# Optimization experiments

Measured on AMD Instinct MI355X. Metric: run time of the kernel, lower is better.

Reference implementation:

```python
import jax, jax.numpy as jnp
import numpy as np

E, D, H = 1024, 64, 16   # embed_dim, head_dim, num_heads
B, L = 8, 4096


def _ln(x, g, b, eps=1e-5):
    m = jnp.mean(x, axis=-1, keepdims=True)
    v = jnp.var(x, axis=-1, keepdims=True)
    return (x - m) / jnp.sqrt(v + eps) * g + b


def setup_inputs() -> dict:
    key = jax.random.key(0)
    ks = jax.random.split(key, 10)
    s_e = 1.0 / np.sqrt(E)
    s_d = 1.0 / np.sqrt(D)
    f32 = jnp.float32
    return {
        "emb": jax.random.normal(ks[0], (B, L, E), f32),
        # per-head linears stacked on a leading head axis
        "Wa": jax.random.normal(ks[1], (H, E, D), f32) * s_e,
        "ba": jnp.zeros((H, D), f32),
        "Wb": jax.random.normal(ks[2], (H, E, D), f32) * s_e,
        "bb": jnp.zeros((H, D), f32),
        "Wc": jax.random.normal(ks[3], (H, D, D), f32) * s_d,
        "bc": jnp.zeros((H, D), f32),
        "head_w": jnp.ones((H,), f32),
        "hn_g": jnp.ones((H, D), f32),
        "hn_b": jnp.zeros((H, D), f32),
        "Wd": jax.random.normal(ks[4], (E, D), f32) * s_e,
        "bd": jnp.zeros((D,), f32),
        "W1": jax.random.normal(ks[5], (D, 4 * D), f32) * s_d,
        "b1": jnp.zeros((4 * D,), f32),
        "W2": jax.random.normal(ks[6], (4 * D, D), f32) * (1.0 / np.sqrt(4 * D)),
        "b2": jnp.zeros((D,), f32),
        "Wp": jax.random.normal(ks[7], (D, D), f32) * s_d,
        "bp": jnp.zeros((D,), f32),
        "ng": jnp.ones((D,), f32),
        "nb": jnp.zeros((D,), f32),
    }


def reference(emb, Wa, ba, Wb, bb, Wc, bc, head_w, hn_g, hn_b,
              Wd, bd, W1, b1, W2, b2, Wp, bp, ng, nb):
    b_sz, seq_len, _ = emb.shape
    n_heads, d_head = ba.shape

    # gates depend only on x_t -> precompute for all t, all heads  [B,L,H,D]
    a = jnp.tanh(jnp.einsum('ble,hed->blhd', emb, Wa) + ba)
    bt = jnp.einsum('ble,hed->blhd', emb, Wb) + bb

    # linear recurrence h_t = a_t * h_{t-1} + b_t over time
    a_t = jnp.moveaxis(a, 1, 0)    # [L,B,H,D]
    b_t = jnp.moveaxis(bt, 1, 0)

    def step(h, ab):
        at, btt = ab
        h = at * h + btt
        return h, h

    h0 = jnp.zeros((b_sz, n_heads, d_head), emb.dtype)
    _, hs = jax.lax.scan(step, h0, (a_t, b_t))
    hs = jnp.moveaxis(hs, 0, 1)    # [B,L,H,D]

    dx = emb @ Wd + bd             # [B,L,D] shared D(x_t)

    out = jnp.einsum('blhd,hde->blhe', hs, Wc) + bc + dx[:, :, None, :]
    out = _ln(out, hn_g, hn_b)     # per-head LayerNorm, gamma/beta [H,D]

    sum_heads = dx + jnp.einsum('h,blhd->bld', head_w, out)
    z = sum_heads / n_heads

    u = z + _ln(z, ng, nb)
    ffn = jax.nn.gelu(u @ W1 + b1, approximate=False) @ W2 + b2
    h_out = u + ffn
    return h_out @ Wp + bp
```

## Files before the change

kernel.cpp:

```cpp
#include <hip/hip_runtime.h>
#include <hip/hip_bf16.h>
#include <math.h>
#include <stdint.h>

#define E_DIM 1024
#define D_DIM 64
#define H_DIM 16
#define B_SZ  8
#define L_SEQ 4096
#define M_TOK (B_SZ * L_SEQ)
#define NCAT  2112
#define NPAD  2304
#define CHUNK 64
#define NCHUNK (L_SEQ / CHUNK)

typedef float  f32x4  __attribute__((ext_vector_type(4)));
typedef __bf16 bf16x8 __attribute__((ext_vector_type(8)));
typedef __bf16 bf16x4 __attribute__((ext_vector_type(4)));

__device__ __forceinline__ float tanh_fast(float v) {
  float vc = fminf(fmaxf(v, -12.f), 12.f);
  float ex = __expf(vc + vc);
  return (ex - 1.f) / (ex + 1.f);
}
__device__ __forceinline__ void load_lds16(const void* g, void* l) {
  __builtin_amdgcn_global_load_lds(
      (const __attribute__((address_space(1))) void*)g,
      (__attribute__((address_space(3))) void*)l, 16, 0, 0);
}

__global__ __launch_bounds__(256) void cast_emb(const float* __restrict__ in,
                                                bf16x4* __restrict__ out) {
  int i = blockIdx.x * 256 + threadIdx.x;
  float4 v = ((const float4*)in)[i];
  bf16x4 o;
  o[0] = (__bf16)v.x; o[1] = (__bf16)v.y; o[2] = (__bf16)v.z; o[3] = (__bf16)v.w;
  out[i] = o;
}

__global__ __launch_bounds__(256) void pack_w(
    const float* __restrict__ Wa, const float* __restrict__ ba,
    const float* __restrict__ Wb, const float* __restrict__ bb,
    const float* __restrict__ Wd, const float* __restrict__ bd,
    __bf16* __restrict__ wcat, float* __restrict__ bias) {
  int gid = blockIdx.x * 256 + threadIdx.x;
  int n = gid >> 10, e = gid & 1023;
  int nt = n >> 8, c = n & 255;
  float w, bv;
  if (nt < 8) {
    int k = nt * 128 + (c >> 1);
    int h = k >> 6, d = k & 63;
    if ((c & 1) == 0) { w = Wa[((h << 10) | e) * 64 + d]; bv = ba[k]; }
    else              { w = Wb[((h << 10) | e) * 64 + d]; bv = bb[k]; }
  } else {
    if (c < 64) { w = Wd[e * 64 + c]; bv = bd[c]; }
    else        { w = 0.f; bv = 0.f; }
  }
  wcat[n * 1024 + e] = (__bf16)w;
  if (e == 0) bias[n] = bv;
}

__global__ __launch_bounds__(256) void pack_ffnw(
    const float* __restrict__ W1, const float* __restrict__ W2,
    const float* __restrict__ Wp,
    __bf16* __restrict__ g_w1t, __bf16* __restrict__ g_w2t,
    __bf16* __restrict__ g_wpt) {
  int idx = blockIdx.x * 256 + threadIdx.x;
  if (idx < 16384) {
    int k = idx >> 8, n = idx & 255;
    g_w1t[n * 72 + k] = (__bf16)W1[idx];
  } else if (idx < 32768) {
    int j = idx - 16384; int k = j >> 6, n = j & 63;
    g_w2t[n * 256 + (((k >> 3) ^ (n & 7)) << 3) + (k & 7)] = (__bf16)W2[j];
  } else {
    int j = idx - 32768; int k = j >> 6, n = j & 63;
    g_wpt[n * 72 + k] = (__bf16)Wp[j];
  }
}

__global__ __launch_bounds__(256) void pack_wct(const float* __restrict__ Wc,
                                                __bf16* __restrict__ wct) {
  int idx = blockIdx.x * 256 + threadIdx.x;
  int h = idx >> 12, e = (idx >> 6) & 63, d = idx & 63;
  wct[idx] = (__bf16)Wc[h * 4096 + d * 64 + e];
}

__global__ __launch_bounds__(512) void gemm_scan_fused(
    const __bf16* __restrict__ A, const __bf16* __restrict__ Wt,
    const float* __restrict__ bias,
    __bf16* __restrict__ abuf, __bf16* __restrict__ bbuf, float* __restrict__ dxbuf,
    float* __restrict__ cA, float* __restrict__ cH) {
  __shared__ __bf16 lds[34816];
  const int id = blockIdx.x;
  const int wg = (id & 7) * 144 + (id >> 3);
  const int mt = wg / 9, nt = wg % 9;
  const int m0 = mt * 256, n0 = nt * 256;
  const int t = threadIdx.x;
  const int w = t >> 6, l = t & 63;
  const int wr = w >> 2, wc = w & 3;
  const int q = l >> 4, c16 = l & 15;
  const int cp = q ^ ((c16 >> 1) & 3);

  f32x4 acc[8][4];
#pragma unroll
  for (int i = 0; i < 8; ++i)
#pragma unroll
    for (int j = 0; j < 4; ++j) acc[i][j] = (f32x4)(0.f);

  auto stage = [&](int kt) {
    const int s = kt & 1;
#pragma unroll
    for (int i = 0; i < 2; ++i) {
      int li = i * 512 + t;
      int rr = li >> 2;
      int lc = (li & 3) ^ ((rr >> 1) & 3);
      load_lds16(A + (size_t)(m0 + rr) * 1024 + kt * 32 + lc * 8,
                 (char*)lds + s * 32768 + li * 16);
      load_lds16(Wt + (size_t)(n0 + rr) * 1024 + kt * 32 + lc * 8,
                 (char*)lds + s * 32768 + 16384 + li * 16);
    }
  };

  stage(0); stage(1);
#pragma unroll 2
  for (int tt = 0; tt < 32; ++tt) {
    if (tt < 31) { asm volatile("s_waitcnt vmcnt(4)" ::: "memory"); }
    else         { asm volatile("s_waitcnt vmcnt(0)" ::: "memory"); }
    __builtin_amdgcn_s_barrier();
    __builtin_amdgcn_sched_barrier(0);
    const __bf16* Abase = lds + (tt & 1) * 16384;
    const __bf16* Bbase = Abase + 8192;
    bf16x8 bfr[4];
#pragma unroll
    for (int j = 0; j < 4; ++j)
      bfr[j] = *(const bf16x8*)(Bbase + (wc * 64 + j * 16 + c16) * 32 + cp * 8);
#pragma unroll
    for (int i = 0; i < 8; ++i) {
      bf16x8 af = *(const bf16x8*)(Abase + (wr * 128 + i * 16 + c16) * 32 + cp * 8);
#pragma unroll
      for (int j = 0; j < 4; ++j)
        acc[i][j] = __builtin_amdgcn_mfma_f32_16x16x32_bf16(af, bfr[j], acc[i][j], 0, 0, 0);
    }
    __builtin_amdgcn_sched_barrier(0);
    __builtin_amdgcn_s_barrier();
    __builtin_amdgcn_sched_barrier(0);
    if (tt < 30) stage(tt + 2);
  }

  const int cbase = m0 >> 6;
  if (nt < 8) {
    float bv4[4];
#pragma unroll
    for (int j = 0; j < 4; ++j) bv4[j] = bias[n0 + wc * 64 + j * 16 + c16];
#pragma unroll 1
    for (int ph = 0; ph < 2; ++ph) {
      __syncthreads();
      if ((wc >> 1) == ph) {
#pragma unroll
        for (int j = 0; j < 4; ++j) {
          int cl = (wc & 1) * 64 + j * 16 + c16;
#pragma unroll
          for (int i = 0; i < 8; ++i) {
            int rowb = wr * 128 + i * 16 + q * 4;
#pragma unroll
            for (int r = 0; r < 4; ++r) {
              float v = acc[i][j][r] + bv4[j];
              float val = (c16 & 1) ? v : tanh_fast(v);
              *(__bf16*)((char*)lds + (rowb + r) * 272 + cl * 2) = (__bf16)val;
            }
          }
        }
      }
      __syncthreads();
      if (t < 256) {
        const int c4 = t >> 6, pp = t & 63;
        const int gk = nt * 128 + ph * 64 + pp;
        const int rb = c4 * 64;
        float p = 1.f, h = 0.f;
        size_t g = (size_t)(m0 + rb) * 1024 + gk;
        const char* lrow = (const char*)lds + rb * 272 + pp * 4;
#pragma unroll 4
        for (int st = 0; st < 64; ++st) {
          float a = (float)*(const __bf16*)(lrow);
          float b = (float)*(const __bf16*)(lrow + 2);
          lrow += 272;
          p *= a;
          h = fmaf(a, h, b);
          abuf[g] = (__bf16)p;
          bbuf[g] = (__bf16)h;
          g += 1024;
        }
        int ci = (cbase + c4) * 1024 + gk;
        cA[ci] = p; cH[ci] = h;
      }
    }
  } else {
    if (wc == 0) {
      float bv4[4];
#pragma unroll
      for (int j = 0; j < 4; ++j) bv4[j] = bias[n0 + j * 16 + c16];
#pragma unroll
      for (int j = 0; j < 4; ++j) {
        int e = j * 16 + c16;
#pragma unroll
        for (int i = 0; i < 8; ++i) {
          int rowb = m0 + wr * 128 + i * 16 + q * 4;
#pragma unroll
          for (int r = 0; r < 4; ++r)
            dxbuf[(size_t)(rowb + r) * 64 + e] = acc[i][j][r] + bv4[j];
        }
      }
    }
  }
}

__global__ __launch_bounds__(256) void scan_carry(
    const float* __restrict__ cA, const float* __restrict__ cH, float* __restrict__ cIn) {
  int gid = blockIdx.x * 256 + threadIdx.x;
  int n = gid & 1023, b = gid >> 10;
  float carry = 0.f;
  for (int c = 0; c < NCHUNK; ++c) {
    int idx = (b * NCHUNK + c) * 1024 + n;
    cIn[idx] = carry;
    carry = fmaf(cA[idx], carry, cH[idx]);
  }
}

__global__ __launch_bounds__(256) void heads_mfma(
    const __bf16* __restrict__ ahat, const __bf16* __restrict__ hloc,
    const float* __restrict__ dxbuf, const float* __restrict__ cIn,
    const __bf16* __restrict__ wct, const float* __restrict__ bch,
    const float* __restrict__ head_w, const float* __restrict__ hng,
    const float* __restrict__ hnb, const float* __restrict__ ng,
    const float* __restrict__ nbv, float* __restrict__ ubuf) {
  __shared__ float carryS[1024];
  const int tid = threadIdx.x, w = tid >> 6, l = tid & 63;
  const int q = l >> 4, c16 = l & 15;
  const int m0 = blockIdx.x * 64;
  const int b = m0 >> 12, c = (m0 & 4095) >> 6;
  const int cb = (b * NCHUNK + c) * 1024;
  ((float4*)carryS)[tid] = ((const float4*)(cIn + cb))[tid];
  __syncthreads();

  const size_t arow = (size_t)(m0 + w * 16 + c16) * 1024;

  float dxr[4][4];
#pragma unroll
  for (int j = 0; j < 4; ++j)
#pragma unroll
    for (int r = 0; r < 4; ++r)
      dxr[j][r] = dxbuf[(m0 + w * 16 + q * 4 + r) * 64 + j * 16 + c16];

  f32x4 accum[4];
#pragma unroll
  for (int j = 0; j < 4; ++j) accum[j] = (f32x4)(0.f);

  for (int h = 0; h < H_DIM; ++h) {
    bf16x8 af[2];
#pragma unroll
    for (int ks = 0; ks < 2; ++ks) {
      int dbase = h * 64 + ks * 32 + q * 8;
      bf16x8 av = *(const bf16x8*)(ahat + arow + dbase);
      bf16x8 hv = *(const bf16x8*)(hloc + arow + dbase);
      float4 cv0 = *(const float4*)(carryS + dbase);
      float4 cv1 = *(const float4*)(carryS + dbase + 4);
      bf16x8 hf;
      hf[0] = (__bf16)fmaf((float)av[0], cv0.x, (float)hv[0]);
      hf[1] = (__bf16)fmaf((float)av[1], cv0.y, (float)hv[1]);
      hf[2] = (__bf16)fmaf((float)av[2], cv0.z, (float)hv[2]);
      hf[3] = (__bf16)fmaf((float)av[3], cv0.w, (float)hv[3]);
      hf[4] = (__bf16)fmaf((float)av[4], cv1.x, (float)hv[4]);
      hf[5] = (__bf16)fmaf((float)av[5], cv1.y, (float)hv[5]);
      hf[6] = (__bf16)fmaf((float)av[6], cv1.z, (float)hv[6]);
      hf[7] = (__bf16)fmaf((float)av[7], cv1.w, (float)hv[7]);
      af[ks] = hf;
    }
    f32x4 acc[4];
#pragma unroll
    for (int j = 0; j < 4; ++j) acc[j] = (f32x4)(0.f);
#pragma unroll
    for (int ks = 0; ks < 2; ++ks)
#pragma unroll
      for (int j = 0; j < 4; ++j) {
        bf16x8 bf = *(const bf16x8*)(wct + h * 4096 + (j * 16 + c16) * 64 + ks * 32 + q * 8);
        acc[j] = __builtin_amdgcn_mfma_f32_16x16x32_bf16(af[ks], bf, acc[j], 0, 0, 0);
      }
    float hw = head_w[h];
    float g4[4], be4[4], bb4[4];
#pragma unroll
    for (int j = 0; j < 4; ++j) {
      int nh = h * 64 + j * 16 + c16;
      g4[j] = hng[nh]; bb4[j] = hnb[nh]; be4[j] = bch[nh];
    }
#pragma unroll
    for (int r = 0; r < 4; ++r) {
      float v0 = acc[0][r] + be4[0] + dxr[0][r];
      float v1 = acc[1][r] + be4[1] + dxr[1][r];
      float v2 = acc[2][r] + be4[2] + dxr[2][r];
      float v3 = acc[3][r] + be4[3] + dxr[3][r];
      float s  = (v0 + v1) + (v2 + v3);
      float s2 = fmaf(v0, v0, fmaf(v1, v1, fmaf(v2, v2, v3 * v3)));
#pragma unroll
      for (int off = 1; off < 16; off <<= 1) {
        s  += __shfl_xor(s, off, 64);
        s2 += __shfl_xor(s2, off, 64);
      }
      float mean = s * (1.f / 64.f);
      float var  = fmaf(s2, 1.f / 64.f, -mean * mean);
      float inv  = rsqrtf(fmaxf(var, 0.f) + 1e-5f);
      accum[0][r] = fmaf(hw, fmaf((v0 - mean) * inv, g4[0], bb4[0]), accum[0][r]);
      accum[1][r] = fmaf(hw, fmaf((v1 - mean) * inv, g4[1], bb4[1]), accum[1][r]);
      accum[2][r] = fmaf(hw, fmaf((v2 - mean) * inv, g4[2], bb4[2]), accum[2][r]);
      accum[3][r] = fmaf(hw, fmaf((v3 - mean) * inv, g4[3], bb4[3]), accum[3][r]);
    }
  }
  float ng4[4], nb4[4];
#pragma unroll
  for (int j = 0; j < 4; ++j) { ng4[j] = ng[j * 16 + c16]; nb4[j] = nbv[j * 16 + c16]; }
#pragma unroll
  for (int r = 0; r < 4; ++r) {
    float z0 = (dxr[0][r] + accum[0][r]) * (1.f / 16.f);
    float z1 = (dxr[1][r] + accum[1][r]) * (1.f / 16.f);
    float z2 = (dxr[2][r] + accum[2][r]) * (1.f / 16.f);
    float z3 = (dxr[3][r] + accum[3][r]) * (1.f / 16.f);
    float s  = (z0 + z1) + (z2 + z3);
    float s2 = fmaf(z0, z0, fmaf(z1, z1, fmaf(z2, z2, z3 * z3)));
#pragma unroll
    for (int off = 1; off < 16; off <<= 1) {
      s  += __shfl_xor(s, off, 64);
      s2 += __shfl_xor(s2, off, 64);
    }
    float mean = s * (1.f / 64.f);
    float var  = fmaf(s2, 1.f / 64.f, -mean * mean);
    float inv  = rsqrtf(fmaxf(var, 0.f) + 1e-5f);
    int mrow = (m0 + w * 16 + q * 4 + r) * 64;
    ubuf[mrow + 0 * 16 + c16] = z0 + fmaf((z0 - mean) * inv, ng4[0], nb4[0]);
    ubuf[mrow + 1 * 16 + c16] = z1 + fmaf((z1 - mean) * inv, ng4[1], nb4[1]);
    ubuf[mrow + 2 * 16 + c16] = z2 + fmaf((z2 - mean) * inv, ng4[2], nb4[2]);
    ubuf[mrow + 3 * 16 + c16] = z3 + fmaf((z3 - mean) * inv, ng4[3], nb4[3]);
  }
}

__global__ __launch_bounds__(256) void ffn_mfma(
    const float* __restrict__ ubuf,
    const __bf16* __restrict__ g_w1t, const __bf16* __restrict__ g_w2t,
    const __bf16* __restrict__ g_wpt,
    const float* __restrict__ b1, const float* __restrict__ b2,
    const float* __restrict__ bp, float* __restrict__ out) {
  __shared__ __bf16 pool[32768];
  const int tid = threadIdx.x, w = tid >> 6, l = tid & 63;
  const int q = l >> 4, c16 = l & 15;
  const int m0 = blockIdx.x * 64;
  __bf16* Us  = pool;
  __bf16* W1T = pool + 4608;
  __bf16* T1S = pool;
  __bf16* W2T = pool + 16384;
  __bf16* HoS = pool;
  __bf16* WpT = pool + 4608;

#pragma unroll
  for (int r = 0; r < 16; ++r) {
    int idx = r * 256 + tid, m = idx >> 6, e = idx & 63;
    Us[m * 72 + e] = (__bf16)ubuf[(size_t)(m0 + m) * 64 + e];
  }
#pragma unroll
  for (int r = 0; r < 9; ++r)
    load_lds16(g_w1t + (size_t)(r * 256 + tid) * 8,
               (char*)pool + 9216 + (r * 256 + w * 64) * 16);
  __syncthreads();

  f32x4 acc1[16];
#pragma unroll
  for (int j = 0; j < 16; ++j) acc1[j] = (f32x4)(0.f);
#pragma unroll
  for (int ks = 0; ks < 2; ++ks) {
    bf16x8 a = *(const bf16x8*)(Us + (w * 16 + c16) * 72 + ks * 32 + q * 8);
#pragma unroll
    for (int j = 0; j < 16; ++j) {
      bf16x8 b = *(const bf16x8*)(W1T + (j * 16 + c16) * 72 + ks * 32 + q * 8);
      acc1[j] = __builtin_amdgcn_mfma_f32_16x16x32_bf16(a, b, acc1[j], 0, 0, 0);
    }
  }
  __syncthreads();

#pragma unroll
  for (int r = 0; r < 8; ++r)
    load_lds16(g_w2t + (size_t)(r * 256 + tid) * 8,
               (char*)pool + 32768 + (r * 256 + w * 64) * 16);
#pragma unroll
  for (int j = 0; j < 16; ++j) {
    int n = j * 16 + c16;
    float bv = b1[n];
#pragma unroll
    for (int rr = 0; rr < 4; ++rr) {
      int m = w * 16 + q * 4 + rr;
      float x = acc1[j][rr] + bv;
      float g = 0.5f * x * (1.f + erff(x * 0.70710678118654752f));
      T1S[m * 256 + (((n >> 3) ^ (m & 7)) << 3) + (n & 7)] = (__bf16)g;
    }
  }
  __syncthreads();

  f32x4 acc2[4];
#pragma unroll
  for (int j = 0; j < 4; ++j) acc2[j] = (f32x4)(0.f);
  const int arow2 = w * 16 + c16;
#pragma unroll
  for (int ks = 0; ks < 8; ++ks) {
    bf16x8 a = *(const bf16x8*)(T1S + arow2 * 256 + (((ks * 4 + q) ^ (arow2 & 7)) << 3));
#pragma unroll
    for (int j = 0; j < 4; ++j) {
      int brow = j * 16 + c16;
      bf16x8 b = *(const bf16x8*)(W2T + brow * 256 + (((ks * 4 + q) ^ (brow & 7)) << 3));
      acc2[j] = __builtin_amdgcn_mfma_f32_16x16x32_bf16(a, b, acc2[j], 0, 0, 0);
    }
  }
  __syncthreads();

#pragma unroll
  for (int r = 0; r < 2; ++r)
    load_lds16(g_wpt + (size_t)(r * 256 + tid) * 8,
               (char*)pool + 9216 + (r * 256 + w * 64) * 16);
  if (tid < 64)
    load_lds16(g_wpt + (size_t)(512 + tid) * 8, (char*)pool + 9216 + 512 * 16);
#pragma unroll
  for (int j = 0; j < 4; ++j) {
    int e = j * 16 + c16;
    float bv = b2[e];
#pragma unroll
    for (int rr = 0; rr < 4; ++rr) {
      int m = w * 16 + q * 4 + rr;
      float hres = acc2[j][rr] + bv + ubuf[(size_t)(m0 + m) * 64 + e];
      HoS[m * 72 + e] = (__bf16)hres;
    }
  }
  __syncthreads();

  f32x4 acc3[4];
#pragma unroll
  for (int j = 0; j < 4; ++j) acc3[j] = (f32x4)(0.f);
#pragma unroll
  for (int ks = 0; ks < 2; ++ks) {
    bf16x8 a = *(const bf16x8*)(HoS + (w * 16 + c16) * 72 + ks * 32 + q * 8);
#pragma unroll
    for (int j = 0; j < 4; ++j) {
      bf16x8 b = *(const bf16x8*)(WpT + (j * 16 + c16) * 72 + ks * 32 + q * 8);
      acc3[j] = __builtin_amdgcn_mfma_f32_16x16x32_bf16(a, b, acc3[j], 0, 0, 0);
    }
  }
#pragma unroll
  for (int j = 0; j < 4; ++j) {
    int e = j * 16 + c16;
    float bv = bp[e];
#pragma unroll
    for (int rr = 0; rr < 4; ++rr) {
      int m = w * 16 + q * 4 + rr;
      out[(size_t)(m0 + m) * 64 + e] = acc3[j][rr] + bv;
    }
  }
}

extern "C" void kernel_launch(void* const* d_in, const int* in_sizes, int n_in,
                              void* d_out, int out_size, void* d_ws, size_t ws_size,
                              hipStream_t stream) {
  const float* emb    = (const float*)d_in[0];
  const float* Wa     = (const float*)d_in[1];
  const float* ba     = (const float*)d_in[2];
  const float* Wb     = (const float*)d_in[3];
  const float* bb     = (const float*)d_in[4];
  const float* Wc     = (const float*)d_in[5];
  const float* bc     = (const float*)d_in[6];
  const float* head_w = (const float*)d_in[7];
  const float* hn_g   = (const float*)d_in[8];
  const float* hn_b   = (const float*)d_in[9];
  const float* Wd     = (const float*)d_in[10];
  const float* bd     = (const float*)d_in[11];
  const float* W1     = (const float*)d_in[12];
  const float* b1     = (const float*)d_in[13];
  const float* W2     = (const float*)d_in[14];
  const float* b2     = (const float*)d_in[15];
  const float* Wp     = (const float*)d_in[16];
  const float* bp     = (const float*)d_in[17];
  const float* ng     = (const float*)d_in[18];
  const float* nb     = (const float*)d_in[19];
  float* out = (float*)d_out;

  char* wsp = (char*)d_ws;
  size_t off = 0;
  auto alloc = [&](size_t bytes) -> char* {
    char* p = wsp + off;
    off += (bytes + 255) & ~(size_t)255;
    return p;
  };
  __bf16* embh  = (__bf16*)alloc((size_t)M_TOK * E_DIM * 2);
  __bf16* wcat  = (__bf16*)alloc((size_t)NPAD * E_DIM * 2);
  float*  bias  = (float*)alloc((size_t)NPAD * 4);
  __bf16* abuf  = (__bf16*)alloc((size_t)M_TOK * 1024 * 2);
  __bf16* bbuf  = (__bf16*)alloc((size_t)M_TOK * 1024 * 2);
  float*  dxbuf = (float*)alloc((size_t)M_TOK * 64 * 4);
  float*  cA    = (float*)alloc((size_t)512 * 1024 * 4);
  float*  cH    = (float*)alloc((size_t)512 * 1024 * 4);
  float*  cIn   = (float*)alloc((size_t)512 * 1024 * 4);
  float*  ubuf  = (float*)alloc((size_t)M_TOK * 64 * 4);
  __bf16* g_w1t = (__bf16*)alloc((size_t)256 * 72 * 2);
  __bf16* g_w2t = (__bf16*)alloc((size_t)64 * 256 * 2);
  __bf16* g_wpt = (__bf16*)alloc((size_t)64 * 72 * 2);
  __bf16* wct   = (__bf16*)alloc((size_t)H_DIM * 64 * 64 * 2);

  cast_emb<<<dim3(32768), dim3(256), 0, stream>>>(emb, (bf16x4*)embh);
  pack_w<<<dim3(9216), dim3(256), 0, stream>>>(Wa, ba, Wb, bb, Wd, bd, wcat, bias);
  pack_ffnw<<<dim3(144), dim3(256), 0, stream>>>(W1, W2, Wp, g_w1t, g_w2t, g_wpt);
  pack_wct<<<dim3(256), dim3(256), 0, stream>>>(Wc, wct);
  gemm_scan_fused<<<dim3(1152), dim3(512), 0, stream>>>(embh, wcat, bias, abuf, bbuf,
                                                        dxbuf, cA, cH);
  scan_carry<<<dim3(32), dim3(256), 0, stream>>>(cA, cH, cIn);
  heads_mfma<<<dim3(512), dim3(256), 0, stream>>>(abuf, bbuf, dxbuf, cIn, wct, bc,
                                                  head_w, hn_g, hn_b, ng, nb, ubuf);
  ffn_mfma<<<dim3(512), dim3(256), 0, stream>>>(ubuf, g_w1t, g_w2t, g_wpt,
                                                b1, b2, bp, out);
}
```

Baseline: 562.5 us.

## Fuse heads and FFN kernels, merge weight packing, batch carry-scan loads

```diff
diff --git a/kernel.cpp b/kernel.cpp
--- a/kernel.cpp
+++ b/kernel.cpp
@@ -38,51 +38,51 @@
   out[i] = o;
 }
 
-__global__ __launch_bounds__(256) void pack_w(
+#define PK0 (NPAD * 1024)
+#define PK1 36864
+#define PK2 65536
+__global__ __launch_bounds__(256) void pack_all(
     const float* __restrict__ Wa, const float* __restrict__ ba,
     const float* __restrict__ Wb, const float* __restrict__ bb,
     const float* __restrict__ Wd, const float* __restrict__ bd,
-    __bf16* __restrict__ wcat, float* __restrict__ bias) {
+    const float* __restrict__ W1, const float* __restrict__ W2,
+    const float* __restrict__ Wp, const float* __restrict__ Wc,
+    __bf16* __restrict__ wcat, float* __restrict__ bias,
+    __bf16* __restrict__ g_w1t, __bf16* __restrict__ g_w2t,
+    __bf16* __restrict__ g_wpt, __bf16* __restrict__ wct) {
   int gid = blockIdx.x * 256 + threadIdx.x;
-  int n = gid >> 10, e = gid & 1023;
-  int nt = n >> 8, c = n & 255;
-  float w, bv;
-  if (nt < 8) {
-    int k = nt * 128 + (c >> 1);
-    int h = k >> 6, d = k & 63;
-    if ((c & 1) == 0) { w = Wa[((h << 10) | e) * 64 + d]; bv = ba[k]; }
-    else              { w = Wb[((h << 10) | e) * 64 + d]; bv = bb[k]; }
+  if (gid < PK0) {
+    int n = gid >> 10, e = gid & 1023;
+    int nt = n >> 8, c = n & 255;
+    float w, bv;
+    if (nt < 8) {
+      int k = nt * 128 + (c >> 1);
+      int h = k >> 6, d = k & 63;
+      if ((c & 1) == 0) { w = Wa[((h << 10) | e) * 64 + d]; bv = ba[k]; }
+      else              { w = Wb[((h << 10) | e) * 64 + d]; bv = bb[k]; }
+    } else {
+      if (c < 64) { w = Wd[e * 64 + c]; bv = bd[c]; }
+      else        { w = 0.f; bv = 0.f; }
+    }
+    wcat[n * 1024 + e] = (__bf16)w;
+    if (e == 0) bias[n] = bv;
+  } else if (gid < PK0 + PK1) {
+    int idx = gid - PK0;
+    if (idx < 16384) {
+      int k = idx >> 8, n = idx & 255;
+      g_w1t[n * 72 + k] = (__bf16)W1[idx];
+    } else if (idx < 32768) {
+      int j = idx - 16384; int k = j >> 6, n = j & 63;
+      g_w2t[n * 256 + (((k >> 3) ^ (n & 7)) << 3) + (k & 7)] = (__bf16)W2[j];
+    } else {
+      int j = idx - 32768; int k = j >> 6, n = j & 63;
+      g_wpt[n * 72 + k] = (__bf16)Wp[j];
+    }
   } else {
-    if (c < 64) { w = Wd[e * 64 + c]; bv = bd[c]; }
-    else        { w = 0.f; bv = 0.f; }
-  }
-  wcat[n * 1024 + e] = (__bf16)w;
-  if (e == 0) bias[n] = bv;
-}
-
-__global__ __launch_bounds__(256) void pack_ffnw(
-    const float* __restrict__ W1, const float* __restrict__ W2,
-    const float* __restrict__ Wp,
-    __bf16* __restrict__ g_w1t, __bf16* __restrict__ g_w2t,
-    __bf16* __restrict__ g_wpt) {
-  int idx = blockIdx.x * 256 + threadIdx.x;
-  if (idx < 16384) {
-    int k = idx >> 8, n = idx & 255;
-    g_w1t[n * 72 + k] = (__bf16)W1[idx];
-  } else if (idx < 32768) {
-    int j = idx - 16384; int k = j >> 6, n = j & 63;
-    g_w2t[n * 256 + (((k >> 3) ^ (n & 7)) << 3) + (k & 7)] = (__bf16)W2[j];
-  } else {
-    int j = idx - 32768; int k = j >> 6, n = j & 63;
-    g_wpt[n * 72 + k] = (__bf16)Wp[j];
-  }
-}
-
-__global__ __launch_bounds__(256) void pack_wct(const float* __restrict__ Wc,
-                                                __bf16* __restrict__ wct) {
-  int idx = blockIdx.x * 256 + threadIdx.x;
-  int h = idx >> 12, e = (idx >> 6) & 63, d = idx & 63;
-  wct[idx] = (__bf16)Wc[h * 4096 + d * 64 + e];
+    int idx = gid - PK0 - PK1;
+    int h = idx >> 12, e = (idx >> 6) & 63, d = idx & 63;
+    wct[idx] = (__bf16)Wc[h * 4096 + d * 64 + e];
+  }
 }
 
 __global__ __launch_bounds__(512) void gemm_scan_fused(
@@ -218,25 +218,52 @@
     const float* __restrict__ cA, const float* __restrict__ cH, float* __restrict__ cIn) {
   int gid = blockIdx.x * 256 + threadIdx.x;
   int n = gid & 1023, b = gid >> 10;
+  const int base = b * NCHUNK * 1024 + n;
   float carry = 0.f;
-  for (int c = 0; c < NCHUNK; ++c) {
-    int idx = (b * NCHUNK + c) * 1024 + n;
-    cIn[idx] = carry;
-    carry = fmaf(cA[idx], carry, cH[idx]);
-  }
-}
-
-__global__ __launch_bounds__(256) void heads_mfma(
+#pragma unroll 1
+  for (int c0 = 0; c0 < NCHUNK; c0 += 8) {
+    float a8[8], h8[8];
+#pragma unroll
+    for (int i = 0; i < 8; ++i) {
+      int idx = base + (c0 + i) * 1024;
+      a8[i] = cA[idx]; h8[i] = cH[idx];
+    }
+#pragma unroll
+    for (int i = 0; i < 8; ++i) {
+      cIn[base + (c0 + i) * 1024] = carry;
+      carry = fmaf(a8[i], carry, h8[i]);
+    }
+  }
+}
+
+__global__ __launch_bounds__(256) void heads_ffn(
     const __bf16* __restrict__ ahat, const __bf16* __restrict__ hloc,
     const float* __restrict__ dxbuf, const float* __restrict__ cIn,
     const __bf16* __restrict__ wct, const float* __restrict__ bch,
     const float* __restrict__ head_w, const float* __restrict__ hng,
     const float* __restrict__ hnb, const float* __restrict__ ng,
-    const float* __restrict__ nbv, float* __restrict__ ubuf) {
-  __shared__ float carryS[1024];
+    const float* __restrict__ nbv,
+    const __bf16* __restrict__ g_w1t, const __bf16* __restrict__ g_w2t,
+    const __bf16* __restrict__ g_wpt,
+    const float* __restrict__ b1, const float* __restrict__ b2,
+    const float* __restrict__ bp, float* __restrict__ out) {
+  __shared__ __bf16 pool[32768];
+  float* carryS = (float*)pool;
   const int tid = threadIdx.x, w = tid >> 6, l = tid & 63;
   const int q = l >> 4, c16 = l & 15;
   const int m0 = blockIdx.x * 64;
+  __bf16* Us  = pool;
+  __bf16* W1T = pool + 4608;
+  __bf16* T1S = pool;
+  __bf16* W2T = pool + 16384;
+  __bf16* HoS = pool;
+  __bf16* WpT = pool + 4608;
+
+#pragma unroll
+  for (int r = 0; r < 9; ++r)
+    load_lds16(g_w1t + (size_t)(r * 256 + tid) * 8,
+               (char*)pool + 9216 + (r * 256 + w * 64) * 16);
+
   const int b = m0 >> 12, c = (m0 & 4095) >> 6;
   const int cb = (b * NCHUNK + c) * 1024;
   ((float4*)carryS)[tid] = ((const float4*)(cIn + cb))[tid];
@@ -314,6 +341,7 @@
       accum[3][r] = fmaf(hw, fmaf((v3 - mean) * inv, g4[3], bb4[3]), accum[3][r]);
     }
   }
+  float u4[4][4];
   float ng4[4], nb4[4];
 #pragma unroll
   for (int j = 0; j < 4; ++j) { ng4[j] = ng[j * 16 + c16]; nb4[j] = nbv[j * 16 + c16]; }
@@ -333,40 +361,17 @@
     float mean = s * (1.f / 64.f);
     float var  = fmaf(s2, 1.f / 64.f, -mean * mean);
     float inv  = rsqrtf(fmaxf(var, 0.f) + 1e-5f);
-    int mrow = (m0 + w * 16 + q * 4 + r) * 64;
-    ubuf[mrow + 0 * 16 + c16] = z0 + fmaf((z0 - mean) * inv, ng4[0], nb4[0]);
-    ubuf[mrow + 1 * 16 + c16] = z1 + fmaf((z1 - mean) * inv, ng4[1], nb4[1]);
-    ubuf[mrow + 2 * 16 + c16] = z2 + fmaf((z2 - mean) * inv, ng4[2], nb4[2]);
-    ubuf[mrow + 3 * 16 + c16] = z3 + fmaf((z3 - mean) * inv, ng4[3], nb4[3]);
-  }
-}
-
-__global__ __launch_bounds__(256) void ffn_mfma(
-    const float* __restrict__ ubuf,
-    const __bf16* __restrict__ g_w1t, const __bf16* __restrict__ g_w2t,
-    const __bf16* __restrict__ g_wpt,
-    const float* __restrict__ b1, const float* __restrict__ b2,
-    const float* __restrict__ bp, float* __restrict__ out) {
-  __shared__ __bf16 pool[32768];
-  const int tid = threadIdx.x, w = tid >> 6, l = tid & 63;
-  const int q = l >> 4, c16 = l & 15;
-  const int m0 = blockIdx.x * 64;
-  __bf16* Us  = pool;
-  __bf16* W1T = pool + 4608;
-  __bf16* T1S = pool;
-  __bf16* W2T = pool + 16384;
-  __bf16* HoS = pool;
-  __bf16* WpT = pool + 4608;
-
-#pragma unroll
-  for (int r = 0; r < 16; ++r) {
-    int idx = r * 256 + tid, m = idx >> 6, e = idx & 63;
-    Us[m * 72 + e] = (__bf16)ubuf[(size_t)(m0 + m) * 64 + e];
-  }
-#pragma unroll
-  for (int r = 0; r < 9; ++r)
-    load_lds16(g_w1t + (size_t)(r * 256 + tid) * 8,
-               (char*)pool + 9216 + (r * 256 + w * 64) * 16);
+    u4[0][r] = z0 + fmaf((z0 - mean) * inv, ng4[0], nb4[0]);
+    u4[1][r] = z1 + fmaf((z1 - mean) * inv, ng4[1], nb4[1]);
+    u4[2][r] = z2 + fmaf((z2 - mean) * inv, ng4[2], nb4[2]);
+    u4[3][r] = z3 + fmaf((z3 - mean) * inv, ng4[3], nb4[3]);
+  }
+  __syncthreads();
+#pragma unroll
+  for (int j = 0; j < 4; ++j)
+#pragma unroll
+    for (int r = 0; r < 4; ++r)
+      Us[(w * 16 + q * 4 + r) * 72 + j * 16 + c16] = (__bf16)u4[j][r];
   __syncthreads();
 
   f32x4 acc1[16];
@@ -377,8 +382,8 @@
     bf16x8 a = *(const bf16x8*)(Us + (w * 16 + c16) * 72 + ks * 32 + q * 8);
 #pragma unroll
     for (int j = 0; j < 16; ++j) {
-      bf16x8 b = *(const bf16x8*)(W1T + (j * 16 + c16) * 72 + ks * 32 + q * 8);
-      acc1[j] = __builtin_amdgcn_mfma_f32_16x16x32_bf16(a, b, acc1[j], 0, 0, 0);
+      bf16x8 bfr = *(const bf16x8*)(W1T + (j * 16 + c16) * 72 + ks * 32 + q * 8);
+      acc1[j] = __builtin_amdgcn_mfma_f32_16x16x32_bf16(a, bfr, acc1[j], 0, 0, 0);
     }
   }
   __syncthreads();
@@ -411,8 +416,8 @@
 #pragma unroll
     for (int j = 0; j < 4; ++j) {
       int brow = j * 16 + c16;
-      bf16x8 b = *(const bf16x8*)(W2T + brow * 256 + (((ks * 4 + q) ^ (brow & 7)) << 3));
-      acc2[j] = __builtin_amdgcn_mfma_f32_16x16x32_bf16(a, b, acc2[j], 0, 0, 0);
+      bf16x8 bfr = *(const bf16x8*)(W2T + brow * 256 + (((ks * 4 + q) ^ (brow & 7)) << 3));
+      acc2[j] = __builtin_amdgcn_mfma_f32_16x16x32_bf16(a, bfr, acc2[j], 0, 0, 0);
     }
   }
   __syncthreads();
@@ -430,7 +435,7 @@
 #pragma unroll
     for (int rr = 0; rr < 4; ++rr) {
       int m = w * 16 + q * 4 + rr;
-      float hres = acc2[j][rr] + bv + ubuf[(size_t)(m0 + m) * 64 + e];
+      float hres = acc2[j][rr] + bv + u4[j][rr];
       HoS[m * 72 + e] = (__bf16)hres;
     }
   }
@@ -444,8 +449,8 @@
     bf16x8 a = *(const bf16x8*)(HoS + (w * 16 + c16) * 72 + ks * 32 + q * 8);
 #pragma unroll
     for (int j = 0; j < 4; ++j) {
-      bf16x8 b = *(const bf16x8*)(WpT + (j * 16 + c16) * 72 + ks * 32 + q * 8);
-      acc3[j] = __builtin_amdgcn_mfma_f32_16x16x32_bf16(a, b, acc3[j], 0, 0, 0);
+      bf16x8 bfr = *(const bf16x8*)(WpT + (j * 16 + c16) * 72 + ks * 32 + q * 8);
+      acc3[j] = __builtin_amdgcn_mfma_f32_16x16x32_bf16(a, bfr, acc3[j], 0, 0, 0);
     }
   }
 #pragma unroll
@@ -501,21 +506,20 @@
   float*  cA    = (float*)alloc((size_t)512 * 1024 * 4);
   float*  cH    = (float*)alloc((size_t)512 * 1024 * 4);
   float*  cIn   = (float*)alloc((size_t)512 * 1024 * 4);
-  float*  ubuf  = (float*)alloc((size_t)M_TOK * 64 * 4);
   __bf16* g_w1t = (__bf16*)alloc((size_t)256 * 72 * 2);
   __bf16* g_w2t = (__bf16*)alloc((size_t)64 * 256 * 2);
   __bf16* g_wpt = (__bf16*)alloc((size_t)64 * 72 * 2);
   __bf16* wct   = (__bf16*)alloc((size_t)H_DIM * 64 * 64 * 2);
 
   cast_emb<<<dim3(32768), dim3(256), 0, stream>>>(emb, (bf16x4*)embh);
-  pack_w<<<dim3(9216), dim3(256), 0, stream>>>(Wa, ba, Wb, bb, Wd, bd, wcat, bias);
-  pack_ffnw<<<dim3(144), dim3(256), 0, stream>>>(W1, W2, Wp, g_w1t, g_w2t, g_wpt);
-  pack_wct<<<dim3(256), dim3(256), 0, stream>>>(Wc, wct);
+  pack_all<<<dim3(9616), dim3(256), 0, stream>>>(Wa, ba, Wb, bb, Wd, bd,
+                                                 W1, W2, Wp, Wc,
+                                                 wcat, bias, g_w1t, g_w2t, g_wpt, wct);
   gemm_scan_fused<<<dim3(1152), dim3(512), 0, stream>>>(embh, wcat, bias, abuf, bbuf,
                                                         dxbuf, cA, cH);
   scan_carry<<<dim3(32), dim3(256), 0, stream>>>(cA, cH, cIn);
-  heads_mfma<<<dim3(512), dim3(256), 0, stream>>>(abuf, bbuf, dxbuf, cIn, wct, bc,
-                                                  head_w, hn_g, hn_b, ng, nb, ubuf);
-  ffn_mfma<<<dim3(512), dim3(256), 0, stream>>>(ubuf, g_w1t, g_w2t, g_wpt,
-                                                b1, b2, bp, out);
-}
+  heads_ffn<<<dim3(512), dim3(256), 0, stream>>>(abuf, bbuf, dxbuf, cIn, wct, bc,
+                                                 head_w, hn_g, hn_b, ng, nb,
+                                                 g_w1t, g_w2t, g_wpt,
+                                                 b1, b2, bp, out);
+}
```

Result: no change. 551.7 us (-1.9%).
